# Optimization experiments

Hardware: AMD Instinct MI355X
Metric: run time of the kernel (lower is better)

Reference implementation:

```python
import jax, jax.numpy as jnp
import numpy as np
from math import pi as PI

K = 32
CUTOFF = 10.0
F = 128          # num_filters (also num_gaussians)
H = 256          # in_channels
N_CLASSES = 7
N_IND = 8
LOG2 = float(np.log(2.0))


def _ssp(x):
    # ShiftedSoftplus
    return jax.nn.softplus(x) - LOG2


def _gaussian_smearing(d):
    # d: [E, 1] -> [E, F]; torch_geometric GaussianSmearing(start=0, stop=cutoff)
    offset = jnp.linspace(0.0, CUTOFF, F, dtype=d.dtype)            # [F]
    coeff = -0.5 / (offset[1] - offset[0]) ** 2
    return jnp.exp(coeff * (d - offset[None, :]) ** 2)


def setup_inputs() -> dict:
    key = jax.random.key(0)
    ks = jax.random.split(key, 24)
    Nq, Nc, B = 8192, 16384, 8
    box = 20.0
    pos_query = jax.random.uniform(ks[0], (Nq, 3), dtype=jnp.float32) * box
    pos_ctx = jax.random.uniform(ks[1], (Nc, 3), dtype=jnp.float32) * box
    node_attr_ctx = jax.random.normal(ks[2], (Nc, H), dtype=jnp.float32)
    batch_query = jnp.sort(jax.random.randint(ks[3], (Nq,), 0, B)).astype(jnp.int32)
    batch_ctx = jnp.sort(jax.random.randint(ks[4], (Nc,), 0, B)).astype(jnp.int32)

    def lin_w(k, fin, fout):
        return (jax.random.normal(k, (fin, fout), dtype=jnp.float32) / np.sqrt(fin)).astype(jnp.float32)

    return {
        "pos_query": pos_query,
        "pos_ctx": pos_ctx,
        "node_attr_ctx": node_attr_ctx,
        "batch_query": batch_query,
        "batch_ctx": batch_ctx,
        "lin1_w": lin_w(ks[5], H, F),                 # bias=False
        "lin2_w": lin_w(ks[6], F, F),
        "lin2_b": jnp.zeros((F,), jnp.float32),
        "nn1_w": lin_w(ks[7], F, F),
        "nn1_b": jnp.zeros((F,), jnp.float32),
        "nn2_w": lin_w(ks[8], F, F),
        "nn2_b": jnp.zeros((F,), jnp.float32),
        "cls1_w": lin_w(ks[9], F, F),
        "cls1_b": jnp.zeros((F,), jnp.float32),
        "cls2_w": lin_w(ks[10], F, N_CLASSES),
        "cls2_b": jnp.zeros((N_CLASSES,), jnp.float32),
        "prop1_w": lin_w(ks[11], F, F),
        "prop1_b": jnp.zeros((F,), jnp.float32),
        "prop2_w": lin_w(ks[12], F, N_IND),
        "prop2_b": jnp.zeros((N_IND,), jnp.float32),
    }


def reference(pos_query, pos_ctx, node_attr_ctx, batch_query, batch_ctx,
              lin1_w, lin2_w, lin2_b, nn1_w, nn1_b, nn2_w, nn2_b,
              cls1_w, cls1_b, cls2_w, cls2_b, prop1_w, prop1_b, prop2_w, prop2_b):
    Nq = pos_query.shape[0]

    # --- batch-aware kNN: for each query, k nearest context points in same graph ---
    d2 = (jnp.sum(pos_query ** 2, -1)[:, None]
          + jnp.sum(pos_ctx ** 2, -1)[None, :]
          - 2.0 * (pos_query @ pos_ctx.T))                            # [Nq, Nc]
    same = batch_query[:, None] == batch_ctx[None, :]
    d2 = jnp.where(same, d2, jnp.inf)
    _, nbr = jax.lax.top_k(-d2, K)                                    # [Nq, K] ctx indices

    # --- gather neighbor data; each query owns exactly K contiguous edges ---
    diff = pos_query[:, None, :] - pos_ctx[nbr]                       # [Nq, K, 3]
    dist = jnp.sqrt(jnp.sum(diff ** 2, -1)).reshape(-1, 1)            # [E, 1]
    attr_j = node_attr_ctx[nbr].reshape(Nq * K, -1)                   # [E, H]

    # --- per-edge filter network on distance expansion ---
    W = _ssp(_gaussian_smearing(dist) @ nn1_w + nn1_b) @ nn2_w + nn2_b  # [E, F]

    h = (W * (attr_j @ lin1_w)) @ lin2_w + lin2_b                     # [E, F]

    # --- cosine cutoff envelope ---
    C = 0.5 * (jnp.cos(dist * (PI / CUTOFF)) + 1.0)
    C = C * (dist <= CUTOFF) * (dist >= 0.0)
    h = h * C                                                         # [E, F]

    # scatter_add by query index == sum over the K contiguous edges per query
    y = jnp.sum(h.reshape(Nq, K, F), axis=1)                          # [Nq, F]

    y_cls = _ssp(y @ cls1_w + cls1_b) @ cls2_w + cls2_b               # [Nq, 7]
    y_ind = _ssp(y @ prop1_w + prop1_b) @ prop2_w + prop2_b           # [Nq, 8]
    return (y_cls, y_ind)
```

## Files before the change

kernel.cpp:

```cpp
#include <hip/hip_runtime.h>
#include <hip/hip_fp16.h>
#include <math.h>

#define K 32
#define F 128
#define H 256
#define TAB 4096
#define QB 8
#define BMAX 16
#define RCUT2 100.0f
#define KBINS 64
#define BINCAP 2560
#define BCAP 128
#define FP 132
#define FRR 32
#define WRR 16

__device__ __forceinline__ float ssp(float x) {
    return fmaxf(x, 0.0f) + log1pf(expf(-fabsf(x))) - 0.69314718055994531f;
}

__device__ __forceinline__ float d2f4(float4 p, float qx, float qy, float qz) {
    float dx = qx - p.x;
    float dy = qy - p.y;
    float dz = qz - p.z;
    return fmaf(dz, dz, fmaf(dy, dy, dx * dx));
}

__global__ __launch_bounds__(256) void prep_kernel(const int* __restrict__ bc, int Nc,
                                                   int* __restrict__ ctx_start,
                                                   const float* __restrict__ posc,
                                                   float4* __restrict__ posc4) {
    int blk = blockIdx.x;
    int tid = threadIdx.x;
    if (blk == 0) {
        if (tid <= BMAX) {
            int b = tid;
            int lo = 0, hi = Nc;
            while (lo < hi) {
                int mid = (lo + hi) >> 1;
                if (bc[mid] < b) lo = mid + 1; else hi = mid;
            }
            ctx_start[b] = lo;
        }
    } else {
        int i = (blk - 1) * 256 + tid;
        if (i < Nc)
            posc4[i] = make_float4(posc[i * 3 + 0], posc[i * 3 + 1], posc[i * 3 + 2], 0.0f);
    }
}

__global__ __launch_bounds__(256) void feat_kernel(const float* __restrict__ attr,
                                                   const float* __restrict__ lin1_w,
                                                   __half* __restrict__ ctx_feat, int Nc) {
    __shared__ float sa[FRR][H];
    int blk = blockIdx.x;
    int tid = threadIdx.x;
    int r0 = blk * FRR;
    int f = tid & 63;
    int g = tid >> 6;

    {
        float4* dst = (float4*)sa;
        const int total = FRR * H / 4;
        if (r0 + FRR <= Nc) {
            const float4* src = (const float4*)(attr + (size_t)r0 * H);
            for (int i = tid; i < total; i += 256) dst[i] = src[i];
        } else {
            for (int i = tid; i < total; i += 256) {
                int r = i / (H / 4);
                if (r0 + r < Nc) dst[i] = ((const float4*)(attr + (size_t)r0 * H))[i];
                else dst[i] = make_float4(0.0f, 0.0f, 0.0f, 0.0f);
            }
        }
    }
    __syncthreads();

    float acc0[8], acc1[8];
#pragma unroll
    for (int r = 0; r < 8; ++r) { acc0[r] = 0.0f; acc1[r] = 0.0f; }
    for (int k = 0; k < H; k += 4) {
        float wa0 = lin1_w[(k + 0) * F + f];
        float wa1 = lin1_w[(k + 1) * F + f];
        float wa2 = lin1_w[(k + 2) * F + f];
        float wa3 = lin1_w[(k + 3) * F + f];
        float wb0 = lin1_w[(k + 0) * F + f + 64];
        float wb1 = lin1_w[(k + 1) * F + f + 64];
        float wb2 = lin1_w[(k + 2) * F + f + 64];
        float wb3 = lin1_w[(k + 3) * F + f + 64];
#pragma unroll
        for (int r = 0; r < 8; ++r) {
            float4 a4 = *(const float4*)&sa[g * 8 + r][k];
            acc0[r] = fmaf(a4.x, wa0, acc0[r]);
            acc0[r] = fmaf(a4.y, wa1, acc0[r]);
            acc0[r] = fmaf(a4.z, wa2, acc0[r]);
            acc0[r] = fmaf(a4.w, wa3, acc0[r]);
            acc1[r] = fmaf(a4.x, wb0, acc1[r]);
            acc1[r] = fmaf(a4.y, wb1, acc1[r]);
            acc1[r] = fmaf(a4.z, wb2, acc1[r]);
            acc1[r] = fmaf(a4.w, wb3, acc1[r]);
        }
    }
#pragma unroll
    for (int r = 0; r < 8; ++r) {
        int row = r0 + g * 8 + r;
        if (row < Nc) {
            ctx_feat[(size_t)row * F + f] = __float2half(acc0[r]);
            ctx_feat[(size_t)row * F + f + 64] = __float2half(acc1[r]);
        }
    }
}

__global__ __launch_bounds__(256) void knn_kernel(const float* __restrict__ posq,
                                                  const float4* __restrict__ posc4,
                                                  const int* __restrict__ bq,
                                                  const int* __restrict__ ctx_start,
                                                  int* __restrict__ nbr, int Nq) {
    __shared__ unsigned char sbin[4][BINCAP];
    __shared__ int hist[4][KBINS];
    __shared__ unsigned bkey[4][BCAP];
    __shared__ int bidx[4][BCAP];
    __shared__ int s_nwin[4], s_nbnd[4];

    int tid = threadIdx.x;
    int lane = tid & 63;
    int w = tid >> 6;
    int q = blockIdx.x * 4 + w;
    bool active = q < Nq;
    int qc = active ? q : 0;

    hist[w][lane] = 0;
    if (lane == 0) { s_nwin[w] = 0; s_nbnd[w] = 0; }

    float qx = posq[qc * 3 + 0];
    float qy = posq[qc * 3 + 1];
    float qz = posq[qc * 3 + 2];
    int b = bq[qc];
    int c0 = ctx_start[b];
    int c1 = ctx_start[b + 1];
    int seg = active ? (c1 - c0) : 0;
    __syncthreads();

    const float SCALE = (float)KBINS / RCUT2;
    int farc = -1;

    for (int i = lane; i < seg; i += 64) {
        float d2 = d2f4(posc4[c0 + i], qx, qy, qz);
        int bin = 255;
        if (d2 < RCUT2) {
            bin = (int)(d2 * SCALE);
            atomicAdd(&hist[w][bin], 1);
        }
        if (i < BINCAP) sbin[w][i] = (unsigned char)bin;
    }
    __syncthreads();

    int h = hist[w][lane];
    int inc = h;
#pragma unroll
    for (int off = 1; off < 64; off <<= 1) {
        int v = __shfl_up(inc, off);
        if (lane >= off) inc += v;
    }
    unsigned long long bal = __ballot(inc >= K);
    int T, below;
    if (bal) {
        T = __ffsll(bal) - 1;
        below = __shfl(inc, T) - __shfl(h, T);
    } else {
        T = KBINS;
        below = __shfl(inc, 63);
    }

    for (int i = lane; i < seg; i += 64) {
        int c = c0 + i;
        int bin;
        if (i < BINCAP) bin = sbin[w][i];
        else {
            float d2 = d2f4(posc4[c], qx, qy, qz);
            bin = (d2 < RCUT2) ? (int)(d2 * SCALE) : 255;
        }
        if (bin < T) {
            int p = atomicAdd(&s_nwin[w], 1);
            nbr[(size_t)q * K + p] = c;
        } else if (bin == T) {
            int p = atomicAdd(&s_nbnd[w], 1);
            if (p < BCAP) {
                float d2 = d2f4(posc4[c], qx, qy, qz);
                bkey[w][p] = __float_as_uint(d2);
                bidx[w][p] = c;
            }
        } else if (bin == 255) {
            farc = c;
        }
    }
#pragma unroll
    for (int off = 1; off < 64; off <<= 1) farc = max(farc, __shfl_xor(farc, off));
    if (farc < 0) farc = c0;
    __syncthreads();

    if (!active) return;
    int nb = min(s_nbnd[w], BCAP);
    int m = K - s_nwin[w];
    for (int it = 0; it < m; ++it) {
        unsigned long long bestkey = 0xFFFFFFFFFFFFFFFFull;
        int bestp = -1;
        for (int p = lane; p < nb; p += 64) {
            unsigned kk = bkey[w][p];
            if (kk != 0xFFFFFFFFu) {
                unsigned long long pk = ((unsigned long long)kk << 32) | (unsigned)bidx[w][p];
                if (pk < bestkey) { bestkey = pk; bestp = p; }
            }
        }
#pragma unroll
        for (int off = 1; off < 64; off <<= 1) {
            unsigned long long ok = __shfl_xor(bestkey, off);
            int op = __shfl_xor(bestp, off);
            if (ok < bestkey) { bestkey = ok; bestp = op; }
        }
        if (lane == 0) {
            if (bestp >= 0 && bestkey != 0xFFFFFFFFFFFFFFFFull) {
                nbr[(size_t)q * K + below + it] = (int)(bestkey & 0xFFFFFFFFu);
                bkey[w][bestp] = 0xFFFFFFFFu;
            } else {
                nbr[(size_t)q * K + below + it] = farc;
            }
        }
        __asm__ volatile("" ::: "memory");
    }
}

__global__ __launch_bounds__(256) void wtab_kernel(const float* __restrict__ nn1_w,
                                                   const float* __restrict__ nn1_b,
                                                   const float* __restrict__ nn2_w,
                                                   const float* __restrict__ nn2_b,
                                                   __half2* __restrict__ wt2h) {
    __shared__ float sg[17][F];
    __shared__ float st[17][F];
    int t0 = blockIdx.x * WRR;
    int tid = threadIdx.x;
    int f = tid & (F - 1);
    int g = tid >> 7;

    const float delta = 10.0f / 127.0f;
    const float coeff = -0.5f / (delta * delta);
    float off = (float)f * delta;
    for (int r = g; r < 17; r += 2) {
        float dist = (float)(t0 + r) * (10.0f / (float)TAB);
        float d = dist - off;
        sg[r][f] = expf(coeff * d * d);
    }
    __syncthreads();

    float acc[9];
#pragma unroll
    for (int r = 0; r < 9; ++r) acc[r] = 0.0f;
    for (int j = 0; j < F; j += 4) {
        float w0 = nn1_w[(j + 0) * F + f];
        float w1 = nn1_w[(j + 1) * F + f];
        float w2 = nn1_w[(j + 2) * F + f];
        float w3 = nn1_w[(j + 3) * F + f];
#pragma unroll
        for (int r = 0; r < 9; ++r) {
            float4 a4 = *(const float4*)&sg[g * 8 + r][j];
            acc[r] = fmaf(a4.x, w0, acc[r]);
            acc[r] = fmaf(a4.y, w1, acc[r]);
            acc[r] = fmaf(a4.z, w2, acc[r]);
            acc[r] = fmaf(a4.w, w3, acc[r]);
        }
    }
    float b1 = nn1_b[f];
#pragma unroll
    for (int r = 0; r < 9; ++r) st[g * 8 + r][f] = ssp(acc[r] + b1);
    __syncthreads();

#pragma unroll
    for (int r = 0; r < 9; ++r) acc[r] = 0.0f;
    for (int j = 0; j < F; j += 4) {
        float w0 = nn2_w[(j + 0) * F + f];
        float w1 = nn2_w[(j + 1) * F + f];
        float w2 = nn2_w[(j + 2) * F + f];
        float w3 = nn2_w[(j + 3) * F + f];
#pragma unroll
        for (int r = 0; r < 9; ++r) {
            float4 a4 = *(const float4*)&st[g * 8 + r][j];
            acc[r] = fmaf(a4.x, w0, acc[r]);
            acc[r] = fmaf(a4.y, w1, acc[r]);
            acc[r] = fmaf(a4.z, w2, acc[r]);
            acc[r] = fmaf(a4.w, w3, acc[r]);
        }
    }
    float b2 = nn2_b[f];
#pragma unroll
    for (int i = 0; i < 8; ++i) {
        int t = t0 + g * 8 + i;
        wt2h[(size_t)t * F + f] = __floats2half2_rn(acc[i] + b2, acc[i + 1] + b2);
    }
}

__global__ __launch_bounds__(256) void agghead_kernel(const float* __restrict__ posq,
                                                      const float4* __restrict__ posc4,
                                                      const int* __restrict__ nbr,
                                                      const __half* __restrict__ ctx_feat,
                                                      const __half2* __restrict__ wt2h,
                                                      const float* __restrict__ lin2_w,
                                                      const float* __restrict__ lin2_b,
                                                      const float* __restrict__ cls1_w,
                                                      const float* __restrict__ cls1_b,
                                                      const float* __restrict__ cls2_w,
                                                      const float* __restrict__ cls2_b,
                                                      const float* __restrict__ prop1_w,
                                                      const float* __restrict__ prop1_b,
                                                      const float* __restrict__ prop2_w,
                                                      const float* __restrict__ prop2_b,
                                                      float* __restrict__ out_cls,
                                                      float* __restrict__ out_ind, int Nq) {
    const int QH = QB / 2;
    int q0 = blockIdx.x * QB;
    int tid = threadIdx.x;

    __shared__ __align__(16) char sm[12672];
    float4* sedge      = (float4*)sm;
    float (*sa)[F]     = (float (*)[F])(sm + 4096);
    float* ssc         = (float*)(sm + 8192);
    float (*sc1)[FP]   = (float (*)[FP])(sm);
    float (*sp1)[FP]   = (float (*)[FP])(sm + 4224);
    float (*sy)[FP]    = (float (*)[FP])(sm + 8448);

    {
        int qq = tid >> 5;
        int q = q0 + qq;
        if (q >= Nq) q = Nq - 1;
        int j = nbr[(size_t)q * K + (tid & 31)];
        float4 p = posc4[j];
        float dx = posq[q * 3 + 0] - p.x;
        float dy = posq[q * 3 + 1] - p.y;
        float dz = posq[q * 3 + 2] - p.z;
        float dist = sqrtf(fmaf(dz, dz, fmaf(dy, dy, dx * dx)));
        float C = 0.0f, fr = 0.0f;
        int i0 = 0;
        if (dist <= 10.0f) {
            C = 0.5f * (cosf(dist * 0.31415926535897931f) + 1.0f);
            float u = dist * ((float)TAB / 10.0f);
            i0 = (int)u;
            if (i0 > TAB - 1) i0 = TAB - 1;
            fr = u - (float)i0;
        }
        sedge[tid] = make_float4(C, fr, __int_as_float(i0 * F), __int_as_float(j * F));
        float cs = C;
#pragma unroll
        for (int off = 1; off < 32; off <<= 1) cs += __shfl_xor(cs, off);
        if ((tid & 31) == 0) ssc[qq] = cs;
    }
    __syncthreads();

    {
        int fp = tid & 63;
        int gg = tid >> 6;
        int f0 = fp * 2;
        const __half2* w2b = wt2h + f0;
        const __half* cfb = ctx_feat + f0;
        float accA[2] = {0.0f, 0.0f};
        float accB[2] = {0.0f, 0.0f};
#pragma unroll 2
        for (int k = 0; k < K; ++k) {
            {
                float4 e4 = sedge[(gg * 2 + 0) * K + k];
                float C = e4.x, fr = e4.y;
                int i0f = __float_as_int(e4.z);
                int jf = __float_as_int(e4.w);
                __half2 h01[2];
                *(float2*)h01 = *(const float2*)(w2b + i0f);
                float2 a2 = __half22float2(*(const __half2*)(cfb + jf));
                float2 wa = __half22float2(h01[0]);
                float2 wb = __half22float2(h01[1]);
                float W0 = fmaf(fr, wa.y - wa.x, wa.x);
                float W1 = fmaf(fr, wb.y - wb.x, wb.x);
                accA[0] = fmaf(C * W0, a2.x, accA[0]);
                accA[1] = fmaf(C * W1, a2.y, accA[1]);
            }
            {
                float4 e4 = sedge[(gg * 2 + 1) * K + k];
                float C = e4.x, fr = e4.y;
                int i0f = __float_as_int(e4.z);
                int jf = __float_as_int(e4.w);
                __half2 h01[2];
                *(float2*)h01 = *(const float2*)(w2b + i0f);
                float2 a2 = __half22float2(*(const __half2*)(cfb + jf));
                float2 wa = __half22float2(h01[0]);
                float2 wb = __half22float2(h01[1]);
                float W0 = fmaf(fr, wa.y - wa.x, wa.x);
                float W1 = fmaf(fr, wb.y - wb.x, wb.x);
                accB[0] = fmaf(C * W0, a2.x, accB[0]);
                accB[1] = fmaf(C * W1, a2.y, accB[1]);
            }
        }
        *(float2*)&sa[gg * 2 + 0][f0] = make_float2(accA[0], accA[1]);
        *(float2*)&sa[gg * 2 + 1][f0] = make_float2(accB[0], accB[1]);
    }
    __syncthreads();

    int f = tid & (F - 1);
    int g = tid >> 7;

    {
        float y[QH];
        float lb = lin2_b[f];
#pragma unroll
        for (int i = 0; i < QH; ++i) y[i] = ssc[g * QH + i] * lb;
        for (int j = 0; j < F; j += 4) {
            float w0 = lin2_w[(j + 0) * F + f];
            float w1 = lin2_w[(j + 1) * F + f];
            float w2 = lin2_w[(j + 2) * F + f];
            float w3 = lin2_w[(j + 3) * F + f];
#pragma unroll
            for (int i = 0; i < QH; ++i) {
                float4 a4 = *(const float4*)&sa[g * QH + i][j];
                y[i] = fmaf(a4.x, w0, y[i]);
                y[i] = fmaf(a4.y, w1, y[i]);
                y[i] = fmaf(a4.z, w2, y[i]);
                y[i] = fmaf(a4.w, w3, y[i]);
            }
        }
#pragma unroll
        for (int i = 0; i < QH; ++i) sy[g * QH + i][f] = y[i];
    }
    __syncthreads();

    {
        float c1[QH], p1[QH];
        float cb = cls1_b[f], pb = prop1_b[f];
#pragma unroll
        for (int i = 0; i < QH; ++i) { c1[i] = cb; p1[i] = pb; }
        for (int j = 0; j < F; j += 4) {
            float wc0 = cls1_w[(j + 0) * F + f];
            float wc1 = cls1_w[(j + 1) * F + f];
            float wc2 = cls1_w[(j + 2) * F + f];
            float wc3 = cls1_w[(j + 3) * F + f];
            float wp0 = prop1_w[(j + 0) * F + f];
            float wp1 = prop1_w[(j + 1) * F + f];
            float wp2 = prop1_w[(j + 2) * F + f];
            float wp3 = prop1_w[(j + 3) * F + f];
#pragma unroll
            for (int i = 0; i < QH; ++i) {
                float4 y4 = *(const float4*)&sy[g * QH + i][j];
                c1[i] = fmaf(y4.x, wc0, c1[i]);
                c1[i] = fmaf(y4.y, wc1, c1[i]);
                c1[i] = fmaf(y4.z, wc2, c1[i]);
                c1[i] = fmaf(y4.w, wc3, c1[i]);
                p1[i] = fmaf(y4.x, wp0, p1[i]);
                p1[i] = fmaf(y4.y, wp1, p1[i]);
                p1[i] = fmaf(y4.z, wp2, p1[i]);
                p1[i] = fmaf(y4.w, wp3, p1[i]);
            }
        }
#pragma unroll
        for (int i = 0; i < QH; ++i) {
            sc1[g * QH + i][f] = ssp(c1[i]);
            sp1[g * QH + i][f] = ssp(p1[i]);
        }
    }
    __syncthreads();

    {
        int qq = tid >> 5;
        int c = tid & 31;
        int q = q0 + qq;
        if (q < Nq && c < 15) {
            if (c < 7) {
                float acc = cls2_b[c];
                for (int j = 0; j < F; ++j) acc = fmaf(sc1[qq][j], cls2_w[j * 7 + c], acc);
                out_cls[(size_t)q * 7 + c] = acc;
            } else {
                int cc = c - 7;
                float acc = prop2_b[cc];
                for (int j = 0; j < F; ++j) acc = fmaf(sp1[qq][j], prop2_w[j * 8 + cc], acc);
                out_ind[(size_t)q * 8 + cc] = acc;
            }
        }
    }
}

extern "C" void kernel_launch(void* const* d_in, const int* in_sizes, int n_in,
                              void* d_out, int out_size, void* d_ws, size_t ws_size,
                              hipStream_t stream) {
    const float* posq   = (const float*)d_in[0];
    const float* posc   = (const float*)d_in[1];
    const float* attr   = (const float*)d_in[2];
    const int*   bq     = (const int*)d_in[3];
    const int*   bc     = (const int*)d_in[4];
    const float* lin1_w = (const float*)d_in[5];
    const float* lin2_w = (const float*)d_in[6];
    const float* lin2_b = (const float*)d_in[7];
    const float* nn1_w  = (const float*)d_in[8];
    const float* nn1_b  = (const float*)d_in[9];
    const float* nn2_w  = (const float*)d_in[10];
    const float* nn2_b  = (const float*)d_in[11];
    const float* cls1_w = (const float*)d_in[12];
    const float* cls1_b = (const float*)d_in[13];
    const float* cls2_w = (const float*)d_in[14];
    const float* cls2_b = (const float*)d_in[15];
    const float* prop1_w = (const float*)d_in[16];
    const float* prop1_b = (const float*)d_in[17];
    const float* prop2_w = (const float*)d_in[18];
    const float* prop2_b = (const float*)d_in[19];
    (void)n_in; (void)out_size; (void)ws_size;

    int Nq = in_sizes[0] / 3;
    int Nc = in_sizes[1] / 3;

    char* ws = (char*)d_ws;
    size_t off = 0;
    auto alloc = [&](size_t bytes) {
        off = (off + 255) & ~(size_t)255;
        void* p = ws + off;
        off += bytes;
        return p;
    };
    int*     ctx_start = (int*)alloc((BMAX + 1) * sizeof(int));
    int*     nbr       = (int*)alloc((size_t)Nq * K * sizeof(int));
    __half*  ctx_feat  = (__half*)alloc((size_t)Nc * F * sizeof(__half));
    __half2* wt2h      = (__half2*)alloc((size_t)TAB * F * sizeof(__half2));
    float4*  posc4     = (float4*)alloc((size_t)Nc * sizeof(float4));

    float* out_cls = (float*)d_out;
    float* out_ind = out_cls + (size_t)Nq * 7;

    int padB  = (Nc + 255) / 256;
    int featB = (Nc + FRR - 1) / FRR;
    int knnB  = (Nq + 3) / 4;
    int wtabB = TAB / WRR;

    prep_kernel<<<dim3(1 + padB), dim3(256), 0, stream>>>(bc, Nc, ctx_start, posc, posc4);
    knn_kernel<<<dim3(knnB), dim3(256), 0, stream>>>(posq, posc4, bq, ctx_start, nbr, Nq);
    feat_kernel<<<dim3(featB), dim3(256), 0, stream>>>(attr, lin1_w, ctx_feat, Nc);
    wtab_kernel<<<dim3(wtabB), dim3(256), 0, stream>>>(nn1_w, nn1_b, nn2_w, nn2_b, wt2h);
    agghead_kernel<<<dim3((Nq + QB - 1) / QB), dim3(256), 0, stream>>>(
        posq, posc4, nbr, ctx_feat, wt2h,
        lin2_w, lin2_b, cls1_w, cls1_b, cls2_w, cls2_b,
        prop1_w, prop1_b, prop2_w, prop2_b, out_cls, out_ind, Nq);
}
```

Before: 125.9 us.

## Compute lin1 context features with fp16 MFMA using pre-swizzled weight fragments

```diff
diff --git a/kernel.cpp b/kernel.cpp
--- a/kernel.cpp
+++ b/kernel.cpp
@@ -13,8 +13,10 @@
 #define BINCAP 2560
 #define BCAP 128
 #define FP 132
-#define FRR 32
 #define WRR 16
+
+typedef _Float16 f16x8 __attribute__((ext_vector_type(8)));
+typedef float f32x4 __attribute__((ext_vector_type(4)));
 
 __device__ __forceinline__ float ssp(float x) {
     return fmaxf(x, 0.0f) + log1pf(expf(-fabsf(x))) - 0.69314718055994531f;
@@ -30,7 +32,12 @@
 __global__ __launch_bounds__(256) void prep_kernel(const int* __restrict__ bc, int Nc,
                                                    int* __restrict__ ctx_start,
                                                    const float* __restrict__ posc,
-                                                   float4* __restrict__ posc4) {
+                                                   float4* __restrict__ posc4,
+                                                   const float* __restrict__ attr,
+                                                   __half* __restrict__ attrh,
+                                                   const float* __restrict__ lin1_w,
+                                                   __half* __restrict__ bfragh,
+                                                   int padB, int convB) {
     int blk = blockIdx.x;
     int tid = threadIdx.x;
     if (blk == 0) {
@@ -43,70 +50,77 @@
             }
             ctx_start[b] = lo;
         }
-    } else {
+    } else if (blk <= padB) {
         int i = (blk - 1) * 256 + tid;
         if (i < Nc)
             posc4[i] = make_float4(posc[i * 3 + 0], posc[i * 3 + 1], posc[i * 3 + 2], 0.0f);
-    }
-}
-
-__global__ __launch_bounds__(256) void feat_kernel(const float* __restrict__ attr,
-                                                   const float* __restrict__ lin1_w,
+    } else if (blk <= padB + convB) {
+        size_t base = ((size_t)(blk - 1 - padB) * 256 + tid) * 8;
+        if (base < (size_t)Nc * H) {
+            float4 v0 = *(const float4*)&attr[base];
+            float4 v1 = *(const float4*)&attr[base + 4];
+            __half2 h[4];
+            h[0] = __floats2half2_rn(v0.x, v0.y);
+            h[1] = __floats2half2_rn(v0.z, v0.w);
+            h[2] = __floats2half2_rn(v1.x, v1.y);
+            h[3] = __floats2half2_rn(v1.z, v1.w);
+            *(float4*)&attrh[base] = *(float4*)h;
+        }
+    } else {
+        int ts = blk - 1 - padB - convB;
+        int t = ts >> 3, s = ts & 7;
+        for (int e = tid; e < 512; e += 256) {
+            int l = e >> 3, j = e & 7;
+            int k = s * 32 + (l >> 4) * 8 + j;
+            int col = (l & 15) + 16 * t;
+            bfragh[(size_t)ts * 512 + e] = __float2half(lin1_w[k * F + col]);
+        }
+    }
+}
+
+__global__ __launch_bounds__(256) void feat_kernel(const __half* __restrict__ attrh_,
+                                                   const __half* __restrict__ bfragh_,
                                                    __half* __restrict__ ctx_feat, int Nc) {
-    __shared__ float sa[FRR][H];
-    int blk = blockIdx.x;
+    const _Float16* attrh = (const _Float16*)attrh_;
+    const _Float16* bfragh = (const _Float16*)bfragh_;
     int tid = threadIdx.x;
-    int r0 = blk * FRR;
-    int f = tid & 63;
-    int g = tid >> 6;
-
-    {
-        float4* dst = (float4*)sa;
-        const int total = FRR * H / 4;
-        if (r0 + FRR <= Nc) {
-            const float4* src = (const float4*)(attr + (size_t)r0 * H);
-            for (int i = tid; i < total; i += 256) dst[i] = src[i];
-        } else {
-            for (int i = tid; i < total; i += 256) {
-                int r = i / (H / 4);
-                if (r0 + r < Nc) dst[i] = ((const float4*)(attr + (size_t)r0 * H))[i];
-                else dst[i] = make_float4(0.0f, 0.0f, 0.0f, 0.0f);
-            }
-        }
-    }
-    __syncthreads();
-
-    float acc0[8], acc1[8];
-#pragma unroll
-    for (int r = 0; r < 8; ++r) { acc0[r] = 0.0f; acc1[r] = 0.0f; }
-    for (int k = 0; k < H; k += 4) {
-        float wa0 = lin1_w[(k + 0) * F + f];
-        float wa1 = lin1_w[(k + 1) * F + f];
-        float wa2 = lin1_w[(k + 2) * F + f];
-        float wa3 = lin1_w[(k + 3) * F + f];
-        float wb0 = lin1_w[(k + 0) * F + f + 64];
-        float wb1 = lin1_w[(k + 1) * F + f + 64];
-        float wb2 = lin1_w[(k + 2) * F + f + 64];
-        float wb3 = lin1_w[(k + 3) * F + f + 64];
-#pragma unroll
-        for (int r = 0; r < 8; ++r) {
-            float4 a4 = *(const float4*)&sa[g * 8 + r][k];
-            acc0[r] = fmaf(a4.x, wa0, acc0[r]);
-            acc0[r] = fmaf(a4.y, wa1, acc0[r]);
-            acc0[r] = fmaf(a4.z, wa2, acc0[r]);
-            acc0[r] = fmaf(a4.w, wa3, acc0[r]);
-            acc1[r] = fmaf(a4.x, wb0, acc1[r]);
-            acc1[r] = fmaf(a4.y, wb1, acc1[r]);
-            acc1[r] = fmaf(a4.z, wb2, acc1[r]);
-            acc1[r] = fmaf(a4.w, wb3, acc1[r]);
-        }
-    }
-#pragma unroll
-    for (int r = 0; r < 8; ++r) {
-        int row = r0 + g * 8 + r;
-        if (row < Nc) {
-            ctx_feat[(size_t)row * F + f] = __float2half(acc0[r]);
-            ctx_feat[(size_t)row * F + f + 64] = __float2half(acc1[r]);
+    int wave = tid >> 6;
+    int lane = tid & 63;
+    int r0 = blockIdx.x * 32;
+
+    f32x4 acc[2][2] = {{{0.f,0.f,0.f,0.f},{0.f,0.f,0.f,0.f}},{{0.f,0.f,0.f,0.f},{0.f,0.f,0.f,0.f}}};
+
+    int arow[2];
+#pragma unroll
+    for (int rt = 0; rt < 2; ++rt) {
+        int row = r0 + rt * 16 + (lane & 15);
+        arow[rt] = (row < Nc) ? row : (Nc - 1);
+    }
+    int kbase = (lane >> 4) * 8;
+
+    for (int s = 0; s < 8; ++s) {
+        f16x8 a0 = *(const f16x8*)(attrh + (size_t)arow[0] * H + s * 32 + kbase);
+        f16x8 a1 = *(const f16x8*)(attrh + (size_t)arow[1] * H + s * 32 + kbase);
+#pragma unroll
+        for (int ct = 0; ct < 2; ++ct) {
+            int t = 2 * wave + ct;
+            f16x8 b = *(const f16x8*)(bfragh + ((size_t)(t * 8 + s) * 64 + lane) * 8);
+            acc[0][ct] = __builtin_amdgcn_mfma_f32_16x16x32_f16(a0, b, acc[0][ct], 0, 0, 0);
+            acc[1][ct] = __builtin_amdgcn_mfma_f32_16x16x32_f16(a1, b, acc[1][ct], 0, 0, 0);
+        }
+    }
+
+#pragma unroll
+    for (int rt = 0; rt < 2; ++rt) {
+#pragma unroll
+        for (int ct = 0; ct < 2; ++ct) {
+            int col = (2 * wave + ct) * 16 + (lane & 15);
+#pragma unroll
+            for (int j = 0; j < 4; ++j) {
+                int row = r0 + rt * 16 + (lane >> 4) * 4 + j;
+                if (row < Nc)
+                    ctx_feat[(size_t)row * F + col] = __float2half(acc[rt][ct][j]);
+            }
         }
     }
 }
@@ -522,18 +536,23 @@
     __half*  ctx_feat  = (__half*)alloc((size_t)Nc * F * sizeof(__half));
     __half2* wt2h      = (__half2*)alloc((size_t)TAB * F * sizeof(__half2));
     float4*  posc4     = (float4*)alloc((size_t)Nc * sizeof(float4));
+    __half*  attrh     = (__half*)alloc((size_t)Nc * H * sizeof(__half));
+    __half*  bfragh    = (__half*)alloc((size_t)64 * 512 * sizeof(__half));
 
     float* out_cls = (float*)d_out;
     float* out_ind = out_cls + (size_t)Nq * 7;
 
     int padB  = (Nc + 255) / 256;
-    int featB = (Nc + FRR - 1) / FRR;
+    int convB = (int)(((size_t)Nc * H / 8 + 255) / 256);
+    int swzB  = 64;
+    int featB = (Nc + 31) / 32;
     int knnB  = (Nq + 3) / 4;
     int wtabB = TAB / WRR;
 
-    prep_kernel<<<dim3(1 + padB), dim3(256), 0, stream>>>(bc, Nc, ctx_start, posc, posc4);
+    prep_kernel<<<dim3(1 + padB + convB + swzB), dim3(256), 0, stream>>>(
+        bc, Nc, ctx_start, posc, posc4, attr, attrh, lin1_w, bfragh, padB, convB);
     knn_kernel<<<dim3(knnB), dim3(256), 0, stream>>>(posq, posc4, bq, ctx_start, nbr, Nq);
-    feat_kernel<<<dim3(featB), dim3(256), 0, stream>>>(attr, lin1_w, ctx_feat, Nc);
+    feat_kernel<<<dim3(featB), dim3(256), 0, stream>>>(attrh, bfragh, ctx_feat, Nc);
     wtab_kernel<<<dim3(wtabB), dim3(256), 0, stream>>>(nn1_w, nn1_b, nn2_w, nn2_b, wt2h);
     agghead_kernel<<<dim3((Nq + QB - 1) / QB), dim3(256), 0, stream>>>(
         posq, posc4, nbr, ctx_feat, wt2h,
```

Measured after the change: 112.5 us. 10.7% less time.
